# Performance work log

Hardware: AMD Instinct MI355X
Metric: run time of the kernel (lower is better)

## Reference

```python
import jax, jax.numpy as jnp
import numpy as np

ALPHA, BETA, GAMMA, IOU_THR = 1.0, 1.0, 1.0, 0.5


def _smooth_l1(d):
    a = jnp.abs(d)
    return jnp.where(a < 1.0, 0.5 * d * d, a - 0.5)


def setup_inputs() -> dict:
    key = jax.random.key(0)
    ks = jax.random.split(key, 8)
    B, A, G = 16, 120000, 32
    # anchors: valid corner-format boxes on a ~1024px image
    cxy = jax.random.uniform(ks[0], (A, 2), jnp.float32, 0.0, 1024.0)
    wh = jax.random.uniform(ks[1], (A, 2), jnp.float32, 16.0, 256.0)
    anchors = jnp.concatenate([cxy - 0.5 * wh, cxy + 0.5 * wh], axis=-1)  # [A,4]
    # gt boxes: jittered copies of random anchors (guarantees some IoU>=0.5 matches)
    gidx = jax.random.randint(ks[2], (B, G), 0, A)
    jitter = jax.random.uniform(ks[3], (B, G, 4), jnp.float32, -2.0, 2.0)
    gt_boxes = anchors[gidx] + jitter  # [B,G,4], w,h stay > 0
    return {
        "pred_cls": jax.random.normal(ks[4], (B, A, 2), jnp.float32),
        "pred_bbox": jax.random.normal(ks[5], (B, A, 4), jnp.float32),
        "pred_landmarks": jax.random.normal(ks[6], (B, A, 10), jnp.float32),
        "anchors": anchors,
        "gt_boxes": gt_boxes,
        "gt_landmarks": jax.random.normal(ks[7], (B, G, 10), jnp.float32),
    }


def reference(pred_cls, pred_bbox, pred_landmarks, anchors, gt_boxes, gt_landmarks):
    B, A, _ = pred_cls.shape
    G = gt_boxes.shape[1]
    # ---- pairwise IoU: anchors [A,4] vs gt_boxes [B,G,4] -> [B,A,G] ----
    a = anchors[None, :, None, :]     # [1,A,1,4]
    g = gt_boxes[:, None, :, :]       # [B,1,G,4]
    iw = jnp.clip(jnp.minimum(a[..., 2], g[..., 2]) - jnp.maximum(a[..., 0], g[..., 0]), 0.0)
    ih = jnp.clip(jnp.minimum(a[..., 3], g[..., 3]) - jnp.maximum(a[..., 1], g[..., 1]), 0.0)
    inter = iw * ih
    area_a = (anchors[:, 2] - anchors[:, 0]) * (anchors[:, 3] - anchors[:, 1])  # [A]
    area_g = (gt_boxes[..., 2] - gt_boxes[..., 0]) * (gt_boxes[..., 3] - gt_boxes[..., 1])  # [B,G]
    iou = inter / (area_a[None, :, None] + area_g[:, None, :] - inter)
    max_iou = iou.max(axis=-1)                 # [B,A]
    matched = iou.argmax(axis=-1)              # [B,A] int
    pos = max_iou >= IOU_THR                   # [B,A] bool
    npos = pos.sum(axis=1).astype(pred_cls.dtype)  # [B]

    # ---- classification: CE against binary target (0/1 class index) ----
    target_cls = pos.astype(jnp.int32)
    logp = jax.nn.log_softmax(pred_cls, axis=-1)  # [B,A,2]
    ce = -jnp.take_along_axis(logp, target_cls[..., None], axis=-1)[..., 0]  # [B,A]
    cls_loss = ce.mean(axis=1).mean()

    # ---- gather matched gt per anchor ----
    midx4 = jnp.broadcast_to(matched[:, :, None], (B, A, 4))
    mboxes = jnp.take_along_axis(gt_boxes, midx4, axis=1)        # [B,A,4]
    midx10 = jnp.broadcast_to(matched[:, :, None], (B, A, 10))
    mldm = jnp.take_along_axis(gt_landmarks, midx10, axis=1)     # [B,A,10]

    aw = anchors[:, 2] - anchors[:, 0]
    ah = anchors[:, 3] - anchors[:, 1]
    acx = anchors[:, 0] + 0.5 * aw
    acy = anchors[:, 1] + 0.5 * ah
    gw = mboxes[..., 2] - mboxes[..., 0]
    gh = mboxes[..., 3] - mboxes[..., 1]
    gcx = mboxes[..., 0] + 0.5 * gw
    gcy = mboxes[..., 1] + 0.5 * gh
    reg_t = jnp.stack([(gcx - acx) / aw, (gcy - acy) / ah,
                       jnp.log(gw / aw), jnp.log(gh / ah)], axis=-1)  # [B,A,4]

    m = pos[..., None].astype(pred_cls.dtype)
    reg_l = (_smooth_l1(pred_bbox - reg_t) * m).sum(axis=(1, 2))       # [B]
    ldm_l = (_smooth_l1(pred_landmarks - mldm) * m).sum(axis=(1, 2))   # [B]
    has = npos > 0
    denom = jnp.maximum(npos, 1.0)
    reg_loss = jnp.where(has, reg_l / (denom * 4.0), 0.0).mean()   # mean SmoothL1 over pos elems, /B
    ldm_loss = jnp.where(has, ldm_l / (denom * 10.0), 0.0).mean()

    total = ALPHA * cls_loss + BETA * reg_loss + GAMMA * ldm_loss
    return (total, cls_loss, reg_loss, ldm_loss)
```

## Files before the change

kernel.cpp:

```cpp
#include <hip/hip_runtime.h>
#include <math.h>

#define AN 120000
#define BN 16
#define GN 32
#define NBX ((AN + 255) / 256)

__device__ __forceinline__ float sl1(float d) {
    float ad = fabsf(d);
    return ad < 1.0f ? 0.5f * d * d : ad - 0.5f;
}

__global__ __launch_bounds__(256) void loss_main(
    const float* __restrict__ pred_cls,
    const float* __restrict__ pred_bbox,
    const float* __restrict__ pred_ldm,
    const float* __restrict__ anchors,
    const float* __restrict__ gt_boxes,
    const float* __restrict__ gt_ldm,
    float* __restrict__ partial)
{
    __shared__ float4 gtb[GN];
    __shared__ float  sg[GN];
    __shared__ float  gl[GN * 11];
    __shared__ float  red[4][4];

    const int b   = blockIdx.y;
    const int tid = threadIdx.x;

    if (tid < GN) {
        float4 box = *(const float4*)(gt_boxes + (b * GN + tid) * 4);
        gtb[tid] = box;
        sg[tid]  = (box.z - box.x) * (box.w - box.y);
        const float* lp = gt_ldm + (b * GN + tid) * 10;
        #pragma unroll
        for (int j = 0; j < 10; ++j) gl[tid * 11 + j] = lp[j];
    }
    __syncthreads();

    const int a = blockIdx.x * 256 + tid;
    float ce = 0.f, np = 0.f, rl = 0.f, ll = 0.f;

    if (a < AN) {
        const float4 an4 = *(const float4*)(anchors + (size_t)a * 4);
        const float sa = (an4.z - an4.x) * (an4.w - an4.y);

        bool anypos = false;
        #pragma unroll
        for (int g = 0; g < GN; ++g) {
            float4 gb = gtb[g];
            float iw = fmaxf(fminf(an4.z, gb.z) - fmaxf(an4.x, gb.x), 0.f);
            float ih = fmaxf(fminf(an4.w, gb.w) - fmaxf(an4.y, gb.y), 0.f);
            float inter = iw * ih;
            float uni = sa + sg[g] - inter;
            anypos = anypos | (inter + inter >= uni);
        }

        float2 pc = *(const float2*)(pred_cls + ((size_t)b * AN + a) * 2);
        float mx  = fmaxf(pc.x, pc.y);
        float lse = mx + logf(expf(pc.x - mx) + expf(pc.y - mx));
        ce = lse - (anypos ? pc.y : pc.x);

        if (anypos) {
            float bi = -1.f, bu = 1.f; int bg = 0;
            #pragma unroll
            for (int g = 0; g < GN; ++g) {
                float4 gb = gtb[g];
                float iw = fmaxf(fminf(an4.z, gb.z) - fmaxf(an4.x, gb.x), 0.f);
                float ih = fmaxf(fminf(an4.w, gb.w) - fmaxf(an4.y, gb.y), 0.f);
                float inter = iw * ih;
                float uni = sa + sg[g] - inter;
                bool upd = inter * bu > bi * uni;
                bi = upd ? inter : bi;
                bu = upd ? uni   : bu;
                bg = upd ? g     : bg;
            }
            np = 1.f;
            float4 gb = gtb[bg];
            float aw = an4.z - an4.x, ah = an4.w - an4.y;
            float acx = an4.x + 0.5f * aw, acy = an4.y + 0.5f * ah;
            float gw = gb.z - gb.x, gh = gb.w - gb.y;
            float gcx = gb.x + 0.5f * gw, gcy = gb.y + 0.5f * gh;
            float t0 = (gcx - acx) / aw;
            float t1 = (gcy - acy) / ah;
            float t2 = logf(gw / aw);
            float t3 = logf(gh / ah);
            const float4 pb = *(const float4*)(pred_bbox + ((size_t)b * AN + a) * 4);
            rl = sl1(pb.x - t0) + sl1(pb.y - t1) + sl1(pb.z - t2) + sl1(pb.w - t3);
            const float* pl = pred_ldm + ((size_t)b * AN + a) * 10;
            float s = 0.f;
            #pragma unroll
            for (int j = 0; j < 10; ++j) s += sl1(pl[j] - gl[bg * 11 + j]);
            ll = s;
        }
    }

    #pragma unroll
    for (int off = 32; off > 0; off >>= 1) {
        ce += __shfl_down(ce, off, 64);
        np += __shfl_down(np, off, 64);
        rl += __shfl_down(rl, off, 64);
        ll += __shfl_down(ll, off, 64);
    }
    const int lane = tid & 63, wid = tid >> 6;
    if (lane == 0) { red[0][wid] = ce; red[1][wid] = np; red[2][wid] = rl; red[3][wid] = ll; }
    __syncthreads();
    if (tid < 4) {
        float s = red[tid][0] + red[tid][1] + red[tid][2] + red[tid][3];
        partial[(size_t)tid * (BN * NBX) + (size_t)b * NBX + blockIdx.x] = s;
    }
}

__global__ __launch_bounds__(256) void reduce_partials(
    const float* __restrict__ partial, float* __restrict__ sums)
{
    const int qb = blockIdx.x;
    const float* p = partial + (size_t)qb * NBX;
    float s = 0.f;
    for (int t = threadIdx.x; t < NBX; t += 256) s += p[t];
    #pragma unroll
    for (int off = 32; off > 0; off >>= 1) s += __shfl_down(s, off, 64);
    __shared__ float red[4];
    if ((threadIdx.x & 63) == 0) red[threadIdx.x >> 6] = s;
    __syncthreads();
    if (threadIdx.x == 0) sums[qb] = red[0] + red[1] + red[2] + red[3];
}

__global__ void finalize(const float* __restrict__ sums, float* __restrict__ out)
{
    if (threadIdx.x == 0 && blockIdx.x == 0) {
        float cls = 0.f, reg = 0.f, ldm = 0.f;
        for (int b = 0; b < BN; ++b) {
            cls += sums[0 * BN + b] / (float)AN;
            float npv = sums[1 * BN + b];
            float denom = fmaxf(npv, 1.f);
            bool has = npv > 0.f;
            reg += has ? sums[2 * BN + b] / (denom * 4.f)  : 0.f;
            ldm += has ? sums[3 * BN + b] / (denom * 10.f) : 0.f;
        }
        cls /= (float)BN; reg /= (float)BN; ldm /= (float)BN;
        out[0] = cls + reg + ldm;
        out[1] = cls;
        out[2] = reg;
        out[3] = ldm;
    }
}

extern "C" void kernel_launch(void* const* d_in, const int* in_sizes, int n_in,
                              void* d_out, int out_size, void* d_ws, size_t ws_size,
                              hipStream_t stream) {
    const float* pred_cls  = (const float*)d_in[0];
    const float* pred_bbox = (const float*)d_in[1];
    const float* pred_ldm  = (const float*)d_in[2];
    const float* anchors   = (const float*)d_in[3];
    const float* gt_boxes  = (const float*)d_in[4];
    const float* gt_ldm    = (const float*)d_in[5];
    float* out = (float*)d_out;

    float* partial = (float*)d_ws;
    float* sums    = partial + 4 * BN * NBX;

    dim3 grid1(NBX, BN);
    loss_main<<<grid1, 256, 0, stream>>>(pred_cls, pred_bbox, pred_ldm,
                                         anchors, gt_boxes, gt_ldm, partial);
    reduce_partials<<<4 * BN, 256, 0, stream>>>(partial, sums);
    finalize<<<1, 64, 0, stream>>>(sums, out);
}
```

Before: 178.9 us.

## Process four anchors per thread, simplify IoU test, fuse reduce and finalize

Each thread now handles four anchors, so every LDS read of a GT box is reused across four IoU computations, and the grid shrinks by four. The positive test becomes 3*inter >= sa+sg, which drops the union subtraction, and the CE and log calls switch to fast __expf/__logf intrinsics. The two-stage partial reduction and the finalize kernel merge into one single-block kernel, removing a launch. In exchange, register pressure rises, fewer blocks are resident, and the fast intrinsics can differ slightly in precision.

```diff
diff --git a/kernel.cpp b/kernel.cpp
--- a/kernel.cpp
+++ b/kernel.cpp
@@ -4,7 +4,10 @@
 #define AN 120000
 #define BN 16
 #define GN 32
-#define NBX ((AN + 255) / 256)
+#define APT 4
+#define BLK 256
+#define TILE (BLK * APT)
+#define NBX ((AN + TILE - 1) / TILE)
 
 __device__ __forceinline__ float sl1(float d) {
     float ad = fabsf(d);
@@ -38,60 +41,83 @@
     }
     __syncthreads();
 
-    const int a = blockIdx.x * 256 + tid;
+    const int base = blockIdx.x * TILE + tid;
+
+    float4 an4[APT];
+    float  sa[APT];
+    bool   val[APT];
+    bool   pos[APT];
+
+    #pragma unroll
+    for (int k = 0; k < APT; ++k) {
+        const int a = base + k * BLK;
+        val[k] = (a < AN);
+        pos[k] = false;
+        if (val[k]) {
+            an4[k] = *(const float4*)(anchors + (size_t)a * 4);
+        } else {
+            an4[k] = make_float4(0.f, 0.f, 0.f, 0.f);
+        }
+        sa[k] = (an4[k].z - an4[k].x) * (an4[k].w - an4[k].y);
+    }
+
+    #pragma unroll
+    for (int g = 0; g < GN; ++g) {
+        const float4 gb = gtb[g];
+        const float  s3 = sg[g];
+        #pragma unroll
+        for (int k = 0; k < APT; ++k) {
+            float iw = fmaxf(fminf(an4[k].z, gb.z) - fmaxf(an4[k].x, gb.x), 0.f);
+            float ih = fmaxf(fminf(an4[k].w, gb.w) - fmaxf(an4[k].y, gb.y), 0.f);
+            float inter = iw * ih;
+            pos[k] = pos[k] | (3.f * inter >= sa[k] + s3);
+        }
+    }
+
     float ce = 0.f, np = 0.f, rl = 0.f, ll = 0.f;
 
-    if (a < AN) {
-        const float4 an4 = *(const float4*)(anchors + (size_t)a * 4);
-        const float sa = (an4.z - an4.x) * (an4.w - an4.y);
-
-        bool anypos = false;
-        #pragma unroll
-        for (int g = 0; g < GN; ++g) {
-            float4 gb = gtb[g];
-            float iw = fmaxf(fminf(an4.z, gb.z) - fmaxf(an4.x, gb.x), 0.f);
-            float ih = fmaxf(fminf(an4.w, gb.w) - fmaxf(an4.y, gb.y), 0.f);
-            float inter = iw * ih;
-            float uni = sa + sg[g] - inter;
-            anypos = anypos | (inter + inter >= uni);
-        }
+    #pragma unroll
+    for (int k = 0; k < APT; ++k) {
+        if (!val[k]) continue;
+        const int a = base + k * BLK;
 
         float2 pc = *(const float2*)(pred_cls + ((size_t)b * AN + a) * 2);
-        float mx  = fmaxf(pc.x, pc.y);
-        float lse = mx + logf(expf(pc.x - mx) + expf(pc.y - mx));
-        ce = lse - (anypos ? pc.y : pc.x);
+        float d  = pc.x - pc.y;
+        float e  = __expf(-fabsf(d));
+        float lse = fmaxf(pc.x, pc.y) + __logf(1.f + e);
+        ce += lse - (pos[k] ? pc.y : pc.x);
 
-        if (anypos) {
+        if (pos[k]) {
             float bi = -1.f, bu = 1.f; int bg = 0;
             #pragma unroll
             for (int g = 0; g < GN; ++g) {
                 float4 gb = gtb[g];
-                float iw = fmaxf(fminf(an4.z, gb.z) - fmaxf(an4.x, gb.x), 0.f);
-                float ih = fmaxf(fminf(an4.w, gb.w) - fmaxf(an4.y, gb.y), 0.f);
+                float iw = fmaxf(fminf(an4[k].z, gb.z) - fmaxf(an4[k].x, gb.x), 0.f);
+                float ih = fmaxf(fminf(an4[k].w, gb.w) - fmaxf(an4[k].y, gb.y), 0.f);
                 float inter = iw * ih;
-                float uni = sa + sg[g] - inter;
+                float uni = sa[k] + sg[g] - inter;
                 bool upd = inter * bu > bi * uni;
                 bi = upd ? inter : bi;
                 bu = upd ? uni   : bu;
                 bg = upd ? g     : bg;
             }
-            np = 1.f;
+            np += 1.f;
             float4 gb = gtb[bg];
-            float aw = an4.z - an4.x, ah = an4.w - an4.y;
-            float acx = an4.x + 0.5f * aw, acy = an4.y + 0.5f * ah;
+            float aw = an4[k].z - an4[k].x, ah = an4[k].w - an4[k].y;
+            float acx = an4[k].x + 0.5f * aw, acy = an4[k].y + 0.5f * ah;
             float gw = gb.z - gb.x, gh = gb.w - gb.y;
             float gcx = gb.x + 0.5f * gw, gcy = gb.y + 0.5f * gh;
             float t0 = (gcx - acx) / aw;
             float t1 = (gcy - acy) / ah;
-            float t2 = logf(gw / aw);
-            float t3 = logf(gh / ah);
+            float t2 = __logf(gw / aw);
+            float t3 = __logf(gh / ah);
             const float4 pb = *(const float4*)(pred_bbox + ((size_t)b * AN + a) * 4);
-            rl = sl1(pb.x - t0) + sl1(pb.y - t1) + sl1(pb.z - t2) + sl1(pb.w - t3);
+            rl += sl1(pb.x - t0) + sl1(pb.y - t1) + sl1(pb.z - t2) + sl1(pb.w - t3);
             const float* pl = pred_ldm + ((size_t)b * AN + a) * 10;
             float s = 0.f;
             #pragma unroll
             for (int j = 0; j < 10; ++j) s += sl1(pl[j] - gl[bg * 11 + j]);
-            ll = s;
+            ll += s;
         }
     }
 
@@ -111,32 +137,31 @@
     }
 }
 
-__global__ __launch_bounds__(256) void reduce_partials(
-    const float* __restrict__ partial, float* __restrict__ sums)
+__global__ __launch_bounds__(256) void reduce_finalize(
+    const float* __restrict__ partial, float* __restrict__ out)
 {
-    const int qb = blockIdx.x;
-    const float* p = partial + (size_t)qb * NBX;
+    __shared__ float rowsum[64];
+    const int tid = threadIdx.x;
+    const int row = tid >> 2;
+    const int sub = tid & 3;
+
     float s = 0.f;
-    for (int t = threadIdx.x; t < NBX; t += 256) s += p[t];
-    #pragma unroll
-    for (int off = 32; off > 0; off >>= 1) s += __shfl_down(s, off, 64);
-    __shared__ float red[4];
-    if ((threadIdx.x & 63) == 0) red[threadIdx.x >> 6] = s;
+    const float* p = partial + (size_t)row * NBX;
+    for (int j = sub; j < NBX; j += 4) s += p[j];
+    s += __shfl_down(s, 1, 64);
+    s += __shfl_down(s, 2, 64);
+    if (sub == 0) rowsum[row] = s;
     __syncthreads();
-    if (threadIdx.x == 0) sums[qb] = red[0] + red[1] + red[2] + red[3];
-}
 
-__global__ void finalize(const float* __restrict__ sums, float* __restrict__ out)
-{
-    if (threadIdx.x == 0 && blockIdx.x == 0) {
+    if (tid == 0) {
         float cls = 0.f, reg = 0.f, ldm = 0.f;
         for (int b = 0; b < BN; ++b) {
-            cls += sums[0 * BN + b] / (float)AN;
-            float npv = sums[1 * BN + b];
-            float denom = fmaxf(npv, 1.f);
+            cls += rowsum[0 * BN + b] / (float)AN;
+            float npv = rowsum[1 * BN + b];
+            float den = fmaxf(npv, 1.f);
             bool has = npv > 0.f;
-            reg += has ? sums[2 * BN + b] / (denom * 4.f)  : 0.f;
-            ldm += has ? sums[3 * BN + b] / (denom * 10.f) : 0.f;
+            reg += has ? rowsum[2 * BN + b] / (den * 4.f)  : 0.f;
+            ldm += has ? rowsum[3 * BN + b] / (den * 10.f) : 0.f;
         }
         cls /= (float)BN; reg /= (float)BN; ldm /= (float)BN;
         out[0] = cls + reg + ldm;
@@ -158,11 +183,9 @@
     float* out = (float*)d_out;
 
     float* partial = (float*)d_ws;
-    float* sums    = partial + 4 * BN * NBX;
 
     dim3 grid1(NBX, BN);
-    loss_main<<<grid1, 256, 0, stream>>>(pred_cls, pred_bbox, pred_ldm,
+    loss_main<<<grid1, BLK, 0, stream>>>(pred_cls, pred_bbox, pred_ldm,
                                          anchors, gt_boxes, gt_ldm, partial);
-    reduce_partials<<<4 * BN, 256, 0, stream>>>(partial, sums);
-    finalize<<<1, 64, 0, stream>>>(sums, out);
+    reduce_finalize<<<1, 256, 0, stream>>>(partial, out);
 }
```

Measured after the change: 257.2 us. 43.8% more time.
